# Performance work log

Hardware: AMD Instinct MI355X
Metric: run time of the kernel (lower is better)

The kernel has to match this reference:

```python
import jax, jax.numpy as jnp
import numpy as np

HID, NH, QLR, KVLR, QK, VH, RH = 7168, 128, 1536, 512, 128, 128, 64
EPS = 1.1920929e-07  # torch.finfo(float32).eps, RMSNorm eps=None default
ROPE_BASE = 10000.0


def _rmsnorm(x, w):
    return x * jax.lax.rsqrt(jnp.mean(x * x, axis=-1, keepdims=True) + EPS) * w


def _rope_tables(seq_len, dim):
    inv_freq = 1.0 / (ROPE_BASE ** (np.arange(0, dim, 2, dtype=np.float32) / dim))
    t = np.arange(seq_len, dtype=np.float32)
    freqs = np.outer(t, inv_freq)          # [S, dim/2]
    emb = np.concatenate([freqs, freqs], -1)  # [S, dim]
    return jnp.asarray(np.cos(emb)), jnp.asarray(np.sin(emb))


def _apply_rope(x, cos, sin):
    # x: [B, H, S, D]; rotate-half convention matching the torch module
    d = x.shape[-1]
    x1, x2 = x[..., : d // 2], x[..., d // 2 :]
    rotated = jnp.concatenate([-x2, x1], axis=-1)
    return x * cos + rotated * sin


def setup_inputs() -> dict:
    key = jax.random.key(0)
    ks = jax.random.split(key, 9)
    def w(k, out_dim, in_dim):
        return jax.random.normal(k, (out_dim, in_dim), jnp.float32) / np.sqrt(in_dim)
    return {
        "hidden_states": jax.random.normal(ks[0], (1, 1024, HID), jnp.float32),
        "w_q_down": w(ks[1], QLR, HID),
        "q_norm_w": jnp.ones((QLR,), jnp.float32),
        "w_q_up": w(ks[2], NH * (QK + RH), QLR),
        "w_kv_down": w(ks[3], KVLR + RH, HID),
        "kv_norm_w": jnp.ones((KVLR,), jnp.float32),
        "w_kv_up": w(ks[4], NH * (QK + VH), KVLR),
        "w_out": w(ks[5], HID, NH * VH),
    }


def reference(hidden_states, w_q_down, q_norm_w, w_q_up, w_kv_down, kv_norm_w, w_kv_up, w_out):
    B, S, _ = hidden_states.shape
    cos, sin = _rope_tables(S, RH)

    # Q path: down -> RMSNorm -> up, split into non-rope / rope parts
    c_q = jnp.einsum("bsh,qh->bsq", hidden_states, w_q_down)            # [B,S,QLR]
    q_cr = jnp.einsum("bsq,oq->bso", _rmsnorm(c_q, q_norm_w), w_q_up)   # [B,S,NH*(QK+RH)]
    q_cr = q_cr.reshape(B, S, NH, QK + RH).transpose(0, 2, 1, 3)        # [B,NH,S,QK+RH]
    q_c, q_r = q_cr[..., :QK], q_cr[..., QK:]

    # KV path: shared latent + MQA rope key
    ckv_kr = jnp.einsum("bsh,oh->bso", hidden_states, w_kv_down)        # [B,S,KVLR+RH]
    c_kv, k_r = ckv_kr[..., :KVLR], ckv_kr[..., KVLR:]
    k_r = k_r[:, None, :, :]                                            # [B,1,S,RH]
    kv = jnp.einsum("bsq,oq->bso", _rmsnorm(c_kv, kv_norm_w), w_kv_up)  # [B,S,NH*(QK+VH)]
    kv = kv.reshape(B, S, NH, QK + VH).transpose(0, 2, 1, 3)            # [B,NH,S,QK+VH]
    k_c, v = kv[..., :QK], kv[..., QK:]

    q_r = _apply_rope(q_r, cos, sin)
    k_r = _apply_rope(k_r, cos, sin)

    q = jnp.concatenate([q_c, q_r], axis=-1)                            # [B,NH,S,QK+RH]
    k = jnp.concatenate([k_c, jnp.broadcast_to(k_r, (B, NH, S, RH))], axis=-1)

    scale = 1.0 / np.sqrt(QK + RH)
    scores = jnp.einsum("bhqd,bhkd->bhqk", q, k) * scale
    attn = jax.nn.softmax(scores, axis=-1)
    o = jnp.einsum("bhqk,bhkd->bhqd", attn, v)                          # [B,NH,S,VH]
    o = o.transpose(0, 2, 1, 3).reshape(B, S, NH * VH)
    return jnp.einsum("bso,ho->bsh", o, w_out)
```

## Files before the change

### kernel.cpp

```cpp
#include <hip/hip_runtime.h>
#include <hip/hip_bf16.h>
#include <math.h>

#define HIDN 7168
#define NHEAD 128
#define QLRANK 1536
#define KVLRANK 512
#define QKD 128
#define VHD 128
#define RHD 64
#define SEQ 1024
#define RMS_EPS 1.1920929e-07f

typedef unsigned short u16;
typedef __attribute__((ext_vector_type(8))) short bf16x8;
typedef __attribute__((ext_vector_type(4))) float f32x4;
typedef __attribute__((ext_vector_type(8))) unsigned short u16x8;

__device__ __forceinline__ u16 f2bf(float f) {
    unsigned int u = __float_as_uint(f);
    unsigned int r = (u + 0x7FFFu + ((u >> 16) & 1u)) >> 16;
    return (u16)r;
}
__device__ __forceinline__ float bf2f(u16 v) {
    return __uint_as_float(((unsigned int)v) << 16);
}

__device__ __forceinline__ void gld_lds16(const u16* g, u16* l) {
    __builtin_amdgcn_global_load_lds(
        (const __attribute__((address_space(1))) unsigned int*)g,
        (__attribute__((address_space(3))) unsigned int*)l,
        16, 0, 0);
}

__global__ __launch_bounds__(256) void f32_to_bf16(const float* __restrict__ in,
                                                   u16* __restrict__ out, long n) {
    long i = ((long)blockIdx.x * blockDim.x + threadIdx.x) * 8;
    long stride = (long)gridDim.x * blockDim.x * 8;
    for (; i < n; i += stride) {
        float4 a = *(const float4*)(in + i);
        float4 b = *(const float4*)(in + i + 4);
        u16x8 o;
        o[0] = f2bf(a.x); o[1] = f2bf(a.y); o[2] = f2bf(a.z); o[3] = f2bf(a.w);
        o[4] = f2bf(b.x); o[5] = f2bf(b.y); o[6] = f2bf(b.z); o[7] = f2bf(b.w);
        *(u16x8*)(out + i) = o;
    }
}

template <int OUT_BF16>
__global__ __launch_bounds__(512) void gemm_bt(const u16* __restrict__ A,
                                               const u16* __restrict__ B,
                                               void* __restrict__ Cv,
                                               int M, int N, int Kslice, long ldk) {
    __shared__ u16 As[2 * 128 * 64];
    __shared__ u16 Bs[2 * 128 * 64];
    const int tid = threadIdx.x;
    const int lane = tid & 63;
    const int w = tid >> 6;
    const int wr = w >> 2, wc = w & 3;
    const int l15 = lane & 15, lg = lane >> 4;
    const int n0 = blockIdx.x * 128;
    const int m0 = blockIdx.y * 128;
    const long kbase = (long)blockIdx.z * Kslice;

    const u16* asrc[2];
    const u16* bsrc[2];
    int aoff[2];
#pragma unroll
    for (int i = 0; i < 2; ++i) {
        int r = (w * 2 + i) * 8 + (lane >> 3);
        int gc = (lane & 7) ^ (r & 7);
        asrc[i] = A + (long)(m0 + r) * ldk + kbase + gc * 8;
        int br = n0 + r; if (br >= N) br = N - 1;
        bsrc[i] = B + (long)br * ldk + kbase + gc * 8;
        aoff[i] = (w * 2 + i) * 512;
    }

    f32x4 acc[4][2];
    const f32x4 z = {0.f, 0.f, 0.f, 0.f};
#pragma unroll
    for (int i = 0; i < 4; ++i)
#pragma unroll
        for (int j = 0; j < 2; ++j) acc[i][j] = z;

    auto stage = [&](int bufi, int kofs) {
#pragma unroll
        for (int i = 0; i < 2; ++i) {
            gld_lds16(asrc[i] + kofs, As + bufi * 8192 + aoff[i]);
            gld_lds16(bsrc[i] + kofs, Bs + bufi * 8192 + aoff[i]);
        }
    };

    const int nsteps = Kslice >> 6;
    stage(0, 0);
    asm volatile("s_waitcnt vmcnt(0)" ::: "memory");
    __builtin_amdgcn_s_barrier();

    int cur = 0;
    for (int t = 0; t < nsteps; ++t) {
        if (t + 1 < nsteps) stage(cur ^ 1, (t + 1) * 64);
        const u16* Ab = As + cur * 8192;
        const u16* Bb = Bs + cur * 8192;
#pragma unroll
        for (int kk = 0; kk < 2; ++kk) {
            bf16x8 a[4], b[2];
#pragma unroll
            for (int i = 0; i < 4; ++i) {
                int row = wr * 64 + i * 16 + l15;
                a[i] = *(const bf16x8*)&Ab[row * 64 + ((kk * 4 + lg) ^ (row & 7)) * 8];
            }
#pragma unroll
            for (int j = 0; j < 2; ++j) {
                int row = wc * 32 + j * 16 + l15;
                b[j] = *(const bf16x8*)&Bb[row * 64 + ((kk * 4 + lg) ^ (row & 7)) * 8];
            }
#pragma unroll
            for (int i = 0; i < 4; ++i)
#pragma unroll
                for (int j = 0; j < 2; ++j)
                    acc[i][j] = __builtin_amdgcn_mfma_f32_16x16x32_bf16(a[i], b[j], acc[i][j], 0, 0, 0);
        }
        asm volatile("s_waitcnt vmcnt(0)" ::: "memory");
        __builtin_amdgcn_s_barrier();
        cur ^= 1;
    }

#pragma unroll
    for (int i = 0; i < 4; ++i)
#pragma unroll
        for (int j = 0; j < 2; ++j)
#pragma unroll
            for (int r = 0; r < 4; ++r) {
                int m = m0 + wr * 64 + i * 16 + lg * 4 + r;
                int n = n0 + wc * 32 + j * 16 + l15;
                if (n < N) {
                    if (OUT_BF16)
                        ((u16*)Cv)[(long)m * N + n] = f2bf(acc[i][j][r]);
                    else
                        ((float*)Cv)[(long)blockIdx.z * M * N + (long)m * N + n] = acc[i][j][r];
                }
            }
}

__global__ __launch_bounds__(256) void reduce_parts(const float* __restrict__ parts,
                                                    float* __restrict__ out,
                                                    int nparts, long mn) {
    long i = ((long)blockIdx.x * 256 + threadIdx.x) * 4;
    long stride = (long)gridDim.x * 256 * 4;
    for (; i < mn; i += stride) {
        float4 s = *(const float4*)(parts + i);
        for (int p = 1; p < nparts; ++p) {
            float4 v = *(const float4*)(parts + (long)p * mn + i);
            s.x += v.x; s.y += v.y; s.z += v.z; s.w += v.w;
        }
        *(float4*)(out + i) = s;
    }
}

__global__ __launch_bounds__(256) void rmsnorm_kernel(const float* __restrict__ x,
                                                      const float* __restrict__ w,
                                                      u16* __restrict__ y,
                                                      int stride, int norm_len) {
    const int row = blockIdx.x;
    const float* xr = x + (long)row * stride;
    float ss = 0.f;
    for (int i = threadIdx.x; i < norm_len; i += 256) {
        float v = xr[i];
        ss += v * v;
    }
#pragma unroll
    for (int off = 32; off > 0; off >>= 1) ss += __shfl_down(ss, off);
    __shared__ float partial[4];
    if ((threadIdx.x & 63) == 0) partial[threadIdx.x >> 6] = ss;
    __syncthreads();
    float tot = partial[0] + partial[1] + partial[2] + partial[3];
    float rs = 1.0f / sqrtf(tot / (float)norm_len + RMS_EPS);
    u16* yr = y + (long)row * norm_len;
    for (int i = threadIdx.x; i < norm_len; i += 256) yr[i] = f2bf(xr[i] * rs * w[i]);
}

__global__ void rope_tables(float* __restrict__ cos_t, float* __restrict__ sin_t) {
    int s = blockIdx.x;
    int i = threadIdx.x;
    float invf = powf(10000.0f, -((float)(2 * i) / 64.0f));
    float ang = (float)s * invf;
    cos_t[s * 32 + i] = cosf(ang);
    sin_t[s * 32 + i] = sinf(ang);
}

__global__ void rope_q(u16* __restrict__ q_cr, const float* __restrict__ cos_t,
                       const float* __restrict__ sin_t) {
    int s = blockIdx.x;
    int h = blockIdx.y * 2 + (threadIdx.x >> 5);
    int i = threadIdx.x & 31;
    u16* base = q_cr + (s * (NHEAD * 192) + h * 192 + QKD);
    float x1 = bf2f(base[i]);
    float x2 = bf2f(base[i + 32]);
    float c = cos_t[s * 32 + i], sn = sin_t[s * 32 + i];
    base[i]      = f2bf(x1 * c - x2 * sn);
    base[i + 32] = f2bf(x2 * c + x1 * sn);
}

__global__ void rope_k(const float* __restrict__ ckv_kr, const float* __restrict__ cos_t,
                       const float* __restrict__ sin_t, u16* __restrict__ kr) {
    int s = blockIdx.x;
    int i = threadIdx.x;
    if (i < 32) {
        const float* base = ckv_kr + (s * 576 + 512);
        float x1 = base[i], x2 = base[i + 32];
        float c = cos_t[s * 32 + i], sn = sin_t[s * 32 + i];
        kr[s * 64 + i]      = f2bf(x1 * c - x2 * sn);
        kr[s * 64 + i + 32] = f2bf(x2 * c + x1 * sn);
    }
}

__global__ __launch_bounds__(256) void build_vt(const u16* __restrict__ kv,
                                                u16* __restrict__ vT) {
    __shared__ u16 vtile[64][136];
    const int h = blockIdx.x, sb = blockIdx.y, s0 = sb * 64;
    const int tid = threadIdx.x;
#pragma unroll
    for (int it = 0; it < 4; ++it) {
        int c = it * 256 + tid;
        int row = c >> 4;
        int off8 = (c & 15) * 8;
        *(u16x8*)&vtile[row][off8] =
            *(const u16x8*)&kv[(s0 + row) * 32768 + h * 256 + 128 + off8];
    }
    __syncthreads();
    const int sl = tid & 63;
    const int dvb = tid >> 6;
#pragma unroll
    for (int it = 0; it < 32; ++it) {
        int dv = dvb + it * 4;
        vT[(h * 128 + dv) * 1024 + s0 + sl] = vtile[sl][dv];
    }
}

__global__ __launch_bounds__(512) void mla_attn(const u16* __restrict__ q_cr,
                                                const u16* __restrict__ kv,
                                                const u16* __restrict__ kr,
                                                const u16* __restrict__ vT,
                                                u16* __restrict__ o_g) {
    __shared__ u16 ks[64][200];
    __shared__ u16 vts[128][72];
    __shared__ u16 p_lds[8][16][72];
    const int qb = blockIdx.x, h = blockIdx.y;
    const int s0q = qb * 128;
    const int tid = threadIdx.x, lane = tid & 63, w = tid >> 6;
    const int l15 = lane & 15, lg = lane >> 4;
    const float scale = 0.07216878364870323f;

    bf16x8 qreg[6];
    {
        const int qrow = s0q + w * 16 + l15;
#pragma unroll
        for (int kk = 0; kk < 6; ++kk)
            qreg[kk] = *(const bf16x8*)&q_cr[qrow * (NHEAD * 192) + h * 192 + kk * 32 + lg * 8];
    }

    const int krow0 = tid >> 4,           koff0 = (tid & 15) * 8;
    const int krow1 = (512 + tid) >> 4,   koff1 = ((512 + tid) & 15) * 8;
    const int rrow  = tid >> 3,           roff  = (tid & 7) * 8;
    const int vdv0  = tid >> 3,           voff0 = (tid & 7) * 8;
    const int vdv1  = (512 + tid) >> 3,   voff1 = ((512 + tid) & 7) * 8;
    const u16* kvp = kv + h * 256;
    const u16* vtp = vT + (long)(h * 128) * 1024;

    u16x8 kreg0, kreg1, krreg, vreg0, vreg1;
    auto load_tile = [&](int s0k) {
        kreg0 = *(const u16x8*)&kvp[(long)(s0k + krow0) * 32768 + koff0];
        kreg1 = *(const u16x8*)&kvp[(long)(s0k + krow1) * 32768 + koff1];
        krreg = *(const u16x8*)&kr[(s0k + rrow) * 64 + roff];
        vreg0 = *(const u16x8*)&vtp[(long)vdv0 * 1024 + s0k + voff0];
        vreg1 = *(const u16x8*)&vtp[(long)vdv1 * 1024 + s0k + voff1];
    };

    f32x4 o_acc[8];
    const f32x4 z = {0.f, 0.f, 0.f, 0.f};
#pragma unroll
    for (int d = 0; d < 8; ++d) o_acc[d] = z;
    float m_r[4], l_r[4];
#pragma unroll
    for (int r = 0; r < 4; ++r) { m_r[r] = -1e30f; l_r[r] = 0.f; }

    load_tile(0);

    for (int kt = 0; kt < 16; ++kt) {
        __syncthreads();
        *(u16x8*)&ks[krow0][koff0]      = kreg0;
        *(u16x8*)&ks[krow1][koff1]      = kreg1;
        *(u16x8*)&ks[rrow][128 + roff]  = krreg;
        *(u16x8*)&vts[vdv0][voff0]      = vreg0;
        *(u16x8*)&vts[vdv1][voff1]      = vreg1;
        __syncthreads();
        if (kt + 1 < 16) load_tile((kt + 1) * 64);

        f32x4 sf[4];
#pragma unroll
        for (int j = 0; j < 4; ++j) sf[j] = z;
        __builtin_amdgcn_s_setprio(1);
#pragma unroll
        for (int kk = 0; kk < 6; ++kk) {
            bf16x8 a = qreg[kk];
#pragma unroll
            for (int j = 0; j < 4; ++j) {
                bf16x8 b = *(const bf16x8*)&ks[j * 16 + l15][kk * 32 + lg * 8];
                sf[j] = __builtin_amdgcn_mfma_f32_16x16x32_bf16(a, b, sf[j], 0, 0, 0);
            }
        }
        __builtin_amdgcn_s_setprio(0);

        float p[4][4];
        float alpha[4];
#pragma unroll
        for (int r = 0; r < 4; ++r) {
            float mx = fmaxf(fmaxf(sf[0][r], sf[1][r]), fmaxf(sf[2][r], sf[3][r]));
#pragma unroll
            for (int off = 1; off < 16; off <<= 1) mx = fmaxf(mx, __shfl_xor(mx, off));
            mx *= scale;
            float mnew = fmaxf(m_r[r], mx);
            alpha[r] = __expf(m_r[r] - mnew);
            float rs = 0.f;
#pragma unroll
            for (int j = 0; j < 4; ++j) {
                float pv = __expf(sf[j][r] * scale - mnew);
                p[j][r] = pv;
                rs += pv;
            }
#pragma unroll
            for (int off = 1; off < 16; off <<= 1) rs += __shfl_xor(rs, off);
            l_r[r] = l_r[r] * alpha[r] + rs;
            m_r[r] = mnew;
        }
#pragma unroll
        for (int d = 0; d < 8; ++d)
#pragma unroll
            for (int r = 0; r < 4; ++r) o_acc[d][r] *= alpha[r];

#pragma unroll
        for (int j = 0; j < 4; ++j)
#pragma unroll
            for (int r = 0; r < 4; ++r)
                p_lds[w][lg * 4 + r][j * 16 + l15] = f2bf(p[j][r]);

        __builtin_amdgcn_s_setprio(1);
#pragma unroll
        for (int kk2 = 0; kk2 < 2; ++kk2) {
            bf16x8 a = *(const bf16x8*)&p_lds[w][l15][kk2 * 32 + lg * 8];
#pragma unroll
            for (int d = 0; d < 8; ++d) {
                bf16x8 b = *(const bf16x8*)&vts[d * 16 + l15][kk2 * 32 + lg * 8];
                o_acc[d] = __builtin_amdgcn_mfma_f32_16x16x32_bf16(a, b, o_acc[d], 0, 0, 0);
            }
        }
        __builtin_amdgcn_s_setprio(0);
    }

#pragma unroll
    for (int d = 0; d < 8; ++d)
#pragma unroll
        for (int r = 0; r < 4; ++r) {
            int srow = s0q + w * 16 + lg * 4 + r;
            float v = o_acc[d][r] / l_r[r];
            o_g[srow * 16384 + h * 128 + d * 16 + l15] = f2bf(v);
        }
}

extern "C" void kernel_launch(void* const* d_in, const int* in_sizes, int n_in,
                              void* d_out, int out_size, void* d_ws, size_t ws_size,
                              hipStream_t stream) {
    const float* hs        = (const float*)d_in[0];
    const float* w_q_down  = (const float*)d_in[1];
    const float* q_norm_w  = (const float*)d_in[2];
    const float* w_q_up    = (const float*)d_in[3];
    const float* w_kv_down = (const float*)d_in[4];
    const float* kv_norm_w = (const float*)d_in[5];
    const float* w_kv_up   = (const float*)d_in[6];
    const float* w_out     = (const float*)d_in[7];
    float* out = (float*)d_out;
    char* ws = (char*)d_ws;

    const size_t SZ_HS   = (size_t)SEQ * HIDN * 2;
    const size_t SZ_KV   = (size_t)SEQ * 32768 * 2;
    const size_t SZ_QCR  = (size_t)SEQ * (NHEAD * 192) * 2;
    const size_t SZ_VT   = (size_t)NHEAD * 128 * 1024 * 2;
    const size_t SZ_WB   = (size_t)24576 * 1536 * 2;
    const size_t SZ_CQ   = (size_t)SEQ * QLRANK * 4;
    const size_t SZ_CQN  = (size_t)SEQ * QLRANK * 2;
    const size_t SZ_CKV  = (size_t)SEQ * 576 * 4;
    const size_t SZ_CKVN = (size_t)SEQ * KVLRANK * 2;
    const size_t SZ_KR   = (size_t)SEQ * 64 * 2;
    const size_t SZ_OG   = (size_t)SEQ * 16384 * 2;
    const size_t SZ_TAB  = (size_t)SEQ * 32 * 4;

    size_t off = 0;
    u16* hs_bf  = (u16*)(ws + off); off += SZ_HS;
    u16* kvb    = (u16*)(ws + off); off += SZ_KV;
    u16* q_cr   = (u16*)(ws + off); off += SZ_QCR;
    u16* vT     = (u16*)(ws + off); off += SZ_VT;
    u16* W_BUF  = (u16*)(ws + off); off += SZ_WB;
    float* parts = (float*)((char*)W_BUF + 33554432);
    u16* wout_bf = (u16*)ws;
    float* c_q    = (float*)(ws + off); off += SZ_CQ;
    u16* cq_n     = (u16*)(ws + off); off += SZ_CQN;
    float* ckv_kr = (float*)(ws + off); off += SZ_CKV;
    u16* ckv_n    = (u16*)(ws + off); off += SZ_CKVN;
    u16* kr       = (u16*)(ws + off); off += SZ_KR;
    u16* o_g      = (u16*)(ws + off); off += SZ_OG;
    float* cos_t  = (float*)(ws + off); off += SZ_TAB;
    float* sin_t  = (float*)(ws + off); off += SZ_TAB;
    (void)in_sizes; (void)n_in; (void)out_size; (void)ws_size;

    rope_tables<<<dim3(SEQ), dim3(32), 0, stream>>>(cos_t, sin_t);
    f32_to_bf16<<<2048, 256, 0, stream>>>(hs, hs_bf, (long)SEQ * HIDN);

    f32_to_bf16<<<2048, 256, 0, stream>>>(w_q_down, W_BUF, (long)QLRANK * HIDN);
    gemm_bt<0><<<dim3(QLRANK / 128, SEQ / 128, 4), 512, 0, stream>>>(hs_bf, W_BUF, parts, SEQ, QLRANK, HIDN / 4, HIDN);
    reduce_parts<<<1024, 256, 0, stream>>>(parts, c_q, 4, (long)SEQ * QLRANK);
    rmsnorm_kernel<<<SEQ, 256, 0, stream>>>(c_q, q_norm_w, cq_n, QLRANK, QLRANK);

    f32_to_bf16<<<2048, 256, 0, stream>>>(w_q_up, W_BUF, (long)24576 * QLRANK);
    gemm_bt<1><<<dim3(24576 / 128, SEQ / 128), 512, 0, stream>>>(cq_n, W_BUF, q_cr, SEQ, 24576, QLRANK, QLRANK);

    f32_to_bf16<<<2048, 256, 0, stream>>>(w_kv_down, W_BUF, (long)576 * HIDN);
    gemm_bt<0><<<dim3(5, SEQ / 128, 8), 512, 0, stream>>>(hs_bf, W_BUF, parts, SEQ, 576, HIDN / 8, HIDN);
    reduce_parts<<<1024, 256, 0, stream>>>(parts, ckv_kr, 8, (long)SEQ * 576);
    rmsnorm_kernel<<<SEQ, 256, 0, stream>>>(ckv_kr, kv_norm_w, ckv_n, 576, KVLRANK);
    rope_k<<<SEQ, 64, 0, stream>>>(ckv_kr, cos_t, sin_t, kr);

    f32_to_bf16<<<2048, 256, 0, stream>>>(w_kv_up, W_BUF, (long)32768 * KVLRANK);
    gemm_bt<1><<<dim3(32768 / 128, SEQ / 128), 512, 0, stream>>>(ckv_n, W_BUF, kvb, SEQ, 32768, KVLRANK, KVLRANK);

    rope_q<<<dim3(SEQ, NHEAD / 2), 64, 0, stream>>>(q_cr, cos_t, sin_t);
    build_vt<<<dim3(NHEAD, SEQ / 64), 256, 0, stream>>>(kvb, vT);

    mla_attn<<<dim3(SEQ / 128, NHEAD), 512, 0, stream>>>(q_cr, kvb, kr, vT, o_g);

    f32_to_bf16<<<4096, 256, 0, stream>>>(w_out, wout_bf, (long)HIDN * 16384);
    gemm_bt<0><<<dim3(HIDN / 128, SEQ / 128), 512, 0, stream>>>(o_g, wout_bf, out, SEQ, HIDN, 16384, 16384);
}
```

Before: 978.2 us.

## Fuse weight fp32-to-bf16 conversions into preceding GEMM and attention kernels

Stops running w_q_up, w_kv_up and w_out conversions as standalone kernels. Each is instead folded into the main loop of an earlier kernel (q_down GEMM, q_up GEMM, attention), which streams fp32 weight chunks and writes bf16 copies alongside its compute. The goal is to hide the bandwidth-bound conversion passes behind compute-bound work. Workspace is rearranged so each converted weight has its own buffer, with a fallback when the workspace is too small. This adds register pressure and memory traffic inside those kernels, and the attention P buffer padding shrinks from 72 to 68.

```diff
diff --git a/kernel.cpp b/kernel.cpp
--- a/kernel.cpp
+++ b/kernel.cpp
@@ -15,6 +15,7 @@
 typedef unsigned short u16;
 typedef __attribute__((ext_vector_type(8))) short bf16x8;
 typedef __attribute__((ext_vector_type(4))) float f32x4;
+typedef __attribute__((ext_vector_type(4))) unsigned short u16x4;
 typedef __attribute__((ext_vector_type(8))) unsigned short u16x8;
 
 __device__ __forceinline__ u16 f2bf(float f) {
@@ -47,11 +48,14 @@
     }
 }
 
-template <int OUT_BF16>
+template <int OUT_BF16, int FCONV>
 __global__ __launch_bounds__(512) void gemm_bt(const u16* __restrict__ A,
                                                const u16* __restrict__ B,
                                                void* __restrict__ Cv,
-                                               int M, int N, int Kslice, long ldk) {
+                                               int M, int N, int Kslice, long ldk,
+                                               const float* __restrict__ cvsrc,
+                                               u16* __restrict__ cvdst,
+                                               long cvtotal) {
     __shared__ u16 As[2 * 128 * 64];
     __shared__ u16 Bs[2 * 128 * 64];
     const int tid = threadIdx.x;
@@ -76,6 +80,19 @@
         aoff[i] = (w * 2 + i) * 512;
     }
 
+    long gbase = 0, gend = 0;
+    int nwin = 0;
+    float4 cva, cvb;
+    long gcur = -1, gprev = -1;
+    if (FCONV) {
+        const int nblocks = gridDim.x * gridDim.y * gridDim.z;
+        const int bl = (blockIdx.z * gridDim.y + blockIdx.y) * gridDim.x + blockIdx.x;
+        long share = (cvtotal + nblocks - 1) / nblocks;
+        gbase = (long)bl * share;
+        gend = gbase + share; if (gend > cvtotal) gend = cvtotal;
+        nwin = (int)((share + 511) >> 9);
+    }
+
     f32x4 acc[4][2];
     const f32x4 z = {0.f, 0.f, 0.f, 0.f};
 #pragma unroll
@@ -99,6 +116,23 @@
     int cur = 0;
     for (int t = 0; t < nsteps; ++t) {
         if (t + 1 < nsteps) stage(cur ^ 1, (t + 1) * 64);
+        if (FCONV) {
+            if (gprev >= 0) {
+                u16x8 o;
+                o[0] = f2bf(cva.x); o[1] = f2bf(cva.y); o[2] = f2bf(cva.z); o[3] = f2bf(cva.w);
+                o[4] = f2bf(cvb.x); o[5] = f2bf(cvb.y); o[6] = f2bf(cvb.z); o[7] = f2bf(cvb.w);
+                *(u16x8*)(cvdst + gprev * 8) = o;
+            }
+            gprev = -1;
+            if (t < nwin) {
+                long g = gbase + (long)t * 512 + tid;
+                if (g < gend) {
+                    cva = *(const float4*)(cvsrc + g * 8);
+                    cvb = *(const float4*)(cvsrc + g * 8 + 4);
+                    gprev = g;
+                }
+            }
+        }
         const u16* Ab = As + cur * 8192;
         const u16* Bb = Bs + cur * 8192;
 #pragma unroll
@@ -123,6 +157,12 @@
         asm volatile("s_waitcnt vmcnt(0)" ::: "memory");
         __builtin_amdgcn_s_barrier();
         cur ^= 1;
+    }
+    if (FCONV && gprev >= 0) {
+        u16x8 o;
+        o[0] = f2bf(cva.x); o[1] = f2bf(cva.y); o[2] = f2bf(cva.z); o[3] = f2bf(cva.w);
+        o[4] = f2bf(cvb.x); o[5] = f2bf(cvb.y); o[6] = f2bf(cvb.z); o[7] = f2bf(cvb.w);
+        *(u16x8*)(cvdst + gprev * 8) = o;
     }
 
 #pragma unroll
@@ -241,10 +281,13 @@
                                                 const u16* __restrict__ kv,
                                                 const u16* __restrict__ kr,
                                                 const u16* __restrict__ vT,
-                                                u16* __restrict__ o_g) {
+                                                u16* __restrict__ o_g,
+                                                const float* __restrict__ wsrc,
+                                                u16* __restrict__ wdst,
+                                                int do_conv) {
     __shared__ u16 ks[64][200];
     __shared__ u16 vts[128][72];
-    __shared__ u16 p_lds[8][16][72];
+    __shared__ u16 p_lds[8][16][68];
     const int qb = blockIdx.x, h = blockIdx.y;
     const int s0q = qb * 128;
     const int tid = threadIdx.x, lane = tid & 63, w = tid >> 6;
@@ -276,6 +319,35 @@
         vreg1 = *(const u16x8*)&vtp[(long)vdv1 * 1024 + s0k + voff1];
     };
 
+    const long cbase = ((long)(h * 8 + qb)) * 16 * 896;
+    float4 cva0, cvb0, cva1, cvb1;
+    const int gi0 = tid;
+    const int gi1 = 512 + tid;
+    auto conv_load = [&](int kt) {
+        long g0 = cbase + (long)kt * 896;
+        long a0 = (g0 + gi0) * 8;
+        cva0 = *(const float4*)(wsrc + a0);
+        cvb0 = *(const float4*)(wsrc + a0 + 4);
+        if (gi1 < 896) {
+            long a1 = (g0 + gi1) * 8;
+            cva1 = *(const float4*)(wsrc + a1);
+            cvb1 = *(const float4*)(wsrc + a1 + 4);
+        }
+    };
+    auto conv_store = [&](int kt) {
+        long g0 = cbase + (long)kt * 896;
+        u16x8 o;
+        o[0] = f2bf(cva0.x); o[1] = f2bf(cva0.y); o[2] = f2bf(cva0.z); o[3] = f2bf(cva0.w);
+        o[4] = f2bf(cvb0.x); o[5] = f2bf(cvb0.y); o[6] = f2bf(cvb0.z); o[7] = f2bf(cvb0.w);
+        *(u16x8*)(wdst + (g0 + gi0) * 8) = o;
+        if (gi1 < 896) {
+            u16x8 o1;
+            o1[0] = f2bf(cva1.x); o1[1] = f2bf(cva1.y); o1[2] = f2bf(cva1.z); o1[3] = f2bf(cva1.w);
+            o1[4] = f2bf(cvb1.x); o1[5] = f2bf(cvb1.y); o1[6] = f2bf(cvb1.z); o1[7] = f2bf(cvb1.w);
+            *(u16x8*)(wdst + (g0 + gi1) * 8) = o1;
+        }
+    };
+
     f32x4 o_acc[8];
     const f32x4 z = {0.f, 0.f, 0.f, 0.f};
 #pragma unroll
@@ -285,6 +357,7 @@
     for (int r = 0; r < 4; ++r) { m_r[r] = -1e30f; l_r[r] = 0.f; }
 
     load_tile(0);
+    if (do_conv) conv_load(0);
 
     for (int kt = 0; kt < 16; ++kt) {
         __syncthreads();
@@ -295,6 +368,11 @@
         *(u16x8*)&vts[vdv1][voff1]      = vreg1;
         __syncthreads();
         if (kt + 1 < 16) load_tile((kt + 1) * 64);
+
+        if (do_conv) {
+            conv_store(kt);
+            if (kt + 1 < 16) conv_load(kt + 1);
+        }
 
         f32x4 sf[4];
 #pragma unroll
@@ -381,62 +459,80 @@
     float* out = (float*)d_out;
     char* ws = (char*)d_ws;
 
-    const size_t SZ_HS   = (size_t)SEQ * HIDN * 2;
     const size_t SZ_KV   = (size_t)SEQ * 32768 * 2;
     const size_t SZ_QCR  = (size_t)SEQ * (NHEAD * 192) * 2;
+    const size_t SZ_KR   = (size_t)SEQ * 64 * 2;
+    const size_t SZ_TAB  = (size_t)SEQ * 32 * 4;
     const size_t SZ_VT   = (size_t)NHEAD * 128 * 1024 * 2;
-    const size_t SZ_WB   = (size_t)24576 * 1536 * 2;
+    const size_t SZ_OG   = (size_t)SEQ * 16384 * 2;
+    const size_t SZ_WOUT = (size_t)HIDN * 16384 * 2;
+    const size_t SZ_WQD  = (size_t)QLRANK * HIDN * 2;
+    const size_t SZ_WQU  = (size_t)24576 * QLRANK * 2;
+    const size_t SZ_WKD  = (size_t)576 * HIDN * 2;
+    const size_t SZ_WKU  = (size_t)32768 * KVLRANK * 2;
+    const size_t SZ_PART = (size_t)4 * SEQ * QLRANK * 4;
+    const size_t SZ_HS   = (size_t)SEQ * HIDN * 2;
     const size_t SZ_CQ   = (size_t)SEQ * QLRANK * 4;
     const size_t SZ_CQN  = (size_t)SEQ * QLRANK * 2;
     const size_t SZ_CKV  = (size_t)SEQ * 576 * 4;
     const size_t SZ_CKVN = (size_t)SEQ * KVLRANK * 2;
-    const size_t SZ_KR   = (size_t)SEQ * 64 * 2;
-    const size_t SZ_OG   = (size_t)SEQ * 16384 * 2;
-    const size_t SZ_TAB  = (size_t)SEQ * 32 * 4;
 
     size_t off = 0;
-    u16* hs_bf  = (u16*)(ws + off); off += SZ_HS;
-    u16* kvb    = (u16*)(ws + off); off += SZ_KV;
-    u16* q_cr   = (u16*)(ws + off); off += SZ_QCR;
-    u16* vT     = (u16*)(ws + off); off += SZ_VT;
-    u16* W_BUF  = (u16*)(ws + off); off += SZ_WB;
-    float* parts = (float*)((char*)W_BUF + 33554432);
-    u16* wout_bf = (u16*)ws;
-    float* c_q    = (float*)(ws + off); off += SZ_CQ;
-    u16* cq_n     = (u16*)(ws + off); off += SZ_CQN;
-    float* ckv_kr = (float*)(ws + off); off += SZ_CKV;
-    u16* ckv_n    = (u16*)(ws + off); off += SZ_CKVN;
-    u16* kr       = (u16*)(ws + off); off += SZ_KR;
-    u16* o_g      = (u16*)(ws + off); off += SZ_OG;
-    float* cos_t  = (float*)(ws + off); off += SZ_TAB;
-    float* sin_t  = (float*)(ws + off); off += SZ_TAB;
-    (void)in_sizes; (void)n_in; (void)out_size; (void)ws_size;
+    u16* kvb     = (u16*)(ws + off); off += SZ_KV;
+    u16* q_cr    = (u16*)(ws + off); off += SZ_QCR;
+    u16* kr      = (u16*)(ws + off); off += SZ_KR;
+    float* cos_t = (float*)(ws + off); off += SZ_TAB;
+    float* sin_t = (float*)(ws + off); off += SZ_TAB;
+    u16* vT      = (u16*)(ws + off); off += SZ_VT;
+    u16* o_g     = (u16*)(ws + off); off += SZ_OG;
+    const size_t live_end = off;
+    u16* wout_bf = (u16*)(ws + live_end);
+    size_t toff = live_end;
+    u16* wqd_bf  = (u16*)(ws + toff); toff += SZ_WQD;
+    u16* wqu_bf  = (u16*)(ws + toff); toff += SZ_WQU;
+    u16* wkd_bf  = (u16*)(ws + toff); toff += SZ_WKD;
+    u16* wku_bf  = (u16*)(ws + toff); toff += SZ_WKU;
+    float* parts = (float*)(ws + toff); toff += SZ_PART;
+    u16* hs_bf    = (u16*)(ws + toff); toff += SZ_HS;
+    float* c_q    = (float*)(ws + toff); toff += SZ_CQ;
+    u16* cq_n     = (u16*)(ws + toff); toff += SZ_CQN;
+    float* ckv_kr = (float*)(ws + toff); toff += SZ_CKV;
+    u16* ckv_n    = (u16*)(ws + toff); toff += SZ_CKVN;
+    const int fuse = (live_end + SZ_WOUT) <= ws_size;
+    (void)in_sizes; (void)n_in; (void)out_size;
 
     rope_tables<<<dim3(SEQ), dim3(32), 0, stream>>>(cos_t, sin_t);
     f32_to_bf16<<<2048, 256, 0, stream>>>(hs, hs_bf, (long)SEQ * HIDN);
 
-    f32_to_bf16<<<2048, 256, 0, stream>>>(w_q_down, W_BUF, (long)QLRANK * HIDN);
-    gemm_bt<0><<<dim3(QLRANK / 128, SEQ / 128, 4), 512, 0, stream>>>(hs_bf, W_BUF, parts, SEQ, QLRANK, HIDN / 4, HIDN);
+    f32_to_bf16<<<2048, 256, 0, stream>>>(w_q_down, wqd_bf, (long)QLRANK * HIDN);
+    gemm_bt<0, 1><<<dim3(QLRANK / 128, SEQ / 128, 4), 512, 0, stream>>>(
+        hs_bf, wqd_bf, parts, SEQ, QLRANK, HIDN / 4, HIDN,
+        w_q_up, wqu_bf, ((long)24576 * QLRANK) / 8);
     reduce_parts<<<1024, 256, 0, stream>>>(parts, c_q, 4, (long)SEQ * QLRANK);
     rmsnorm_kernel<<<SEQ, 256, 0, stream>>>(c_q, q_norm_w, cq_n, QLRANK, QLRANK);
 
-    f32_to_bf16<<<2048, 256, 0, stream>>>(w_q_up, W_BUF, (long)24576 * QLRANK);
-    gemm_bt<1><<<dim3(24576 / 128, SEQ / 128), 512, 0, stream>>>(cq_n, W_BUF, q_cr, SEQ, 24576, QLRANK, QLRANK);
-
-    f32_to_bf16<<<2048, 256, 0, stream>>>(w_kv_down, W_BUF, (long)576 * HIDN);
-    gemm_bt<0><<<dim3(5, SEQ / 128, 8), 512, 0, stream>>>(hs_bf, W_BUF, parts, SEQ, 576, HIDN / 8, HIDN);
+    gemm_bt<1, 1><<<dim3(24576 / 128, SEQ / 128), 512, 0, stream>>>(
+        cq_n, wqu_bf, q_cr, SEQ, 24576, QLRANK, QLRANK,
+        w_kv_up, wku_bf, ((long)32768 * KVLRANK) / 8);
+
+    f32_to_bf16<<<2048, 256, 0, stream>>>(w_kv_down, wkd_bf, (long)576 * HIDN);
+    gemm_bt<0, 0><<<dim3(5, SEQ / 128, 8), 512, 0, stream>>>(
+        hs_bf, wkd_bf, parts, SEQ, 576, HIDN / 8, HIDN, nullptr, nullptr, 0);
     reduce_parts<<<1024, 256, 0, stream>>>(parts, ckv_kr, 8, (long)SEQ * 576);
     rmsnorm_kernel<<<SEQ, 256, 0, stream>>>(ckv_kr, kv_norm_w, ckv_n, 576, KVLRANK);
     rope_k<<<SEQ, 64, 0, stream>>>(ckv_kr, cos_t, sin_t, kr);
 
-    f32_to_bf16<<<2048, 256, 0, stream>>>(w_kv_up, W_BUF, (long)32768 * KVLRANK);
-    gemm_bt<1><<<dim3(32768 / 128, SEQ / 128), 512, 0, stream>>>(ckv_n, W_BUF, kvb, SEQ, 32768, KVLRANK, KVLRANK);
+    gemm_bt<1, 0><<<dim3(32768 / 128, SEQ / 128), 512, 0, stream>>>(
+        ckv_n, wku_bf, kvb, SEQ, 32768, KVLRANK, KVLRANK, nullptr, nullptr, 0);
 
     rope_q<<<dim3(SEQ, NHEAD / 2), 64, 0, stream>>>(q_cr, cos_t, sin_t);
     build_vt<<<dim3(NHEAD, SEQ / 64), 256, 0, stream>>>(kvb, vT);
 
-    mla_attn<<<dim3(SEQ / 128, NHEAD), 512, 0, stream>>>(q_cr, kvb, kr, vT, o_g);
-
-    f32_to_bf16<<<4096, 256, 0, stream>>>(w_out, wout_bf, (long)HIDN * 16384);
-    gemm_bt<0><<<dim3(HIDN / 128, SEQ / 128), 512, 0, stream>>>(o_g, wout_bf, out, SEQ, HIDN, 16384, 16384);
-}
+    if (!fuse)
+        f32_to_bf16<<<4096, 256, 0, stream>>>(w_out, wout_bf, (long)HIDN * 16384);
+    mla_attn<<<dim3(SEQ / 128, NHEAD), 512, 0, stream>>>(q_cr, kvb, kr, vT, o_g,
+                                                         w_out, wout_bf, fuse ? 1 : 0);
+
+    gemm_bt<0, 0><<<dim3(HIDN / 128, SEQ / 128), 512, 0, stream>>>(
+        o_g, wout_bf, out, SEQ, HIDN, 16384, 16384, nullptr, nullptr, 0);
+}
```

Result: faster. 897.4 us (-8.3%).
